# Optimization experiments

Measured on AMD Instinct MI355X. Metric: run time of the kernel, lower is better.

## Reference

```python
import jax, jax.numpy as jnp
import numpy as np

DIL = 1  # dilation (== padding for 3x3 stride-1)
KK = 9   # 3x3 kernel points


def setup_inputs() -> dict:
    key = jax.random.key(0)
    k1, k2, k3, k4 = jax.random.split(key, 4)
    B, C, H, W = 8, 64, 128, 128
    Cout = 64
    x = jax.random.normal(k1, (B, C, H, W), jnp.float32)
    # offset/mask conv: nn.Conv2d default init scale-ish; keep offsets moderate
    w_off = jax.random.normal(k2, (27, C, 3, 3), jnp.float32) * 0.02
    b_off = jax.random.uniform(k3, (27,), jnp.float32, -0.05, 0.05)
    # c2_msra_fill: std = sqrt(2 / (fan_in + fan_out)), fan_in = C*9
    std = float(np.sqrt(2.0 / (C * 9 + Cout)))
    w_dcn = jax.random.normal(k4, (Cout, C, 3, 3), jnp.float32) * std
    return {"x": x, "w_off": w_off, "b_off": b_off, "w_dcn": w_dcn}


def _conv3x3(x, w, b, dil):
    out = jax.lax.conv_general_dilated(
        x, w, window_strides=(1, 1), padding=[(dil, dil), (dil, dil)],
        rhs_dilation=(dil, dil), dimension_numbers=("NCHW", "OIHW", "NCHW"))
    return out + b[None, :, None, None]


def reference(x, w_off, b_off, w_dcn):
    B, C, H, W = x.shape
    Cout = w_dcn.shape[0]
    # offset/mask conv, chunk into offset_x / offset_y / mask, cat offsets
    om = _conv3x3(x, w_off, b_off, DIL)                  # [B,27,H,W]
    off_x, off_y, mask = jnp.split(om, 3, axis=1)        # each [B,9,H,W]
    offset = jnp.concatenate([off_x, off_y], axis=1)     # [B,18,H,W]
    mask = jax.nn.sigmoid(mask)                          # [B,9,H,W]
    # mmcv DCNv2 layout: offset channel 2k = dy_k, 2k+1 = dx_k
    off = offset.reshape(B, KK, 2, H, W)
    dy, dx = off[:, :, 0], off[:, :, 1]                  # [B,9,H,W]
    # base sampling grid: p = out_pos - pad + k*dil (stride 1, pad = dil)
    ky, kx = jnp.meshgrid(jnp.arange(3), jnp.arange(3), indexing="ij")
    ky = ky.reshape(KK).astype(jnp.float32)
    kx = kx.reshape(KK).astype(jnp.float32)
    base_y = (jnp.arange(H, dtype=jnp.float32)[None, :, None]
              - DIL + ky[:, None, None] * DIL)           # [9,H,1]
    base_x = (jnp.arange(W, dtype=jnp.float32)[None, None, :]
              - DIL + kx[:, None, None] * DIL)           # [9,1,W]
    py = dy + base_y[None]                               # [B,9,H,W]
    px = dx + base_x[None]
    # bilinear sample with zero padding outside the image
    y0 = jnp.floor(py)
    x0 = jnp.floor(px)
    xf = x.reshape(B, C, H * W)
    sampled = jnp.zeros((B, C, KK, H, W), x.dtype)
    for oy in (0.0, 1.0):
        for ox in (0.0, 1.0):
            yi = y0 + oy
            xi = x0 + ox
            wgt = (1.0 - jnp.abs(py - yi)) * (1.0 - jnp.abs(px - xi))
            valid = (yi >= 0) & (yi < H) & (xi >= 0) & (xi < W)
            yc = jnp.clip(yi, 0, H - 1).astype(jnp.int32)
            xc = jnp.clip(xi, 0, W - 1).astype(jnp.int32)
            idx = (yc * W + xc).reshape(B, KK * H * W)
            vals = jax.vmap(lambda f, i: jnp.take(f, i, axis=1))(xf, idx)
            vals = vals.reshape(B, C, KK, H, W)
            sampled = sampled + vals * (wgt * valid)[:, None]
    sampled = sampled * mask[:, None]                    # modulation
    # weighted reduction == conv with gathered patches
    out = jnp.einsum("bckhw,ock->bohw", sampled, w_dcn.reshape(Cout, C, KK))
    return out
```

## Files before the change

kernel.cpp:

```cpp
#include <hip/hip_runtime.h>
#include <math.h>

#define B_  8
#define C_  64
#define H_  128
#define W_  128
#define KK_ 9
#define CO_ 64
#define HW_ (H_*W_)
#define CK_ 576

typedef _Float16 f16x8 __attribute__((ext_vector_type(8)));
typedef _Float16 h2    __attribute__((ext_vector_type(2)));
typedef __attribute__((ext_vector_type(4))) float f32x4;

__device__ inline unsigned pkrtz(float a, float b){
    auto v = __builtin_amdgcn_cvt_pkrtz(a, b);
    union{decltype(v) h; unsigned u;} c; c.h = v; return c.u;
}
__device__ inline h2 u2h(unsigned u){ union{unsigned x; h2 h;} c; c.x = u; return c.h; }
__device__ inline unsigned h2u(h2 v){ union{h2 h; unsigned u;} c; c.h = v; return c.u; }
__device__ inline unsigned short f2h(float f){
    _Float16 h = (_Float16)f;
    union{_Float16 h; unsigned short s;} c; c.h = h; return c.s;
}
__device__ inline h2 bcast_lo(unsigned u){ return u2h(__builtin_amdgcn_perm(u, u, 0x01000100)); }
__device__ inline h2 bcast_hi(unsigned u){ return u2h(__builtin_amdgcn_perm(u, u, 0x03020302)); }

__global__ __launch_bounds__(256) void transpose_prep(
    const float* __restrict__ x, unsigned short* __restrict__ xt,
    const float* __restrict__ w_dcn, const float* __restrict__ w_off,
    unsigned short* __restrict__ w_bf, unsigned short* __restrict__ wA)
{
    __shared__ unsigned tb[64 * 33];
    if (blockIdx.x >= B_ * 256) {
        int i = (blockIdx.x - B_ * 256) * 256 + threadIdx.x;
        if (i < 64 * CK_) {
            int o = i / CK_, r = i % CK_;
            int tap = r >> 6, c = r & 63;
            w_bf[i] = f2h(w_dcn[o * CK_ + c * 9 + tap]);
        } else {
            int j = i - 64 * CK_;
            int o = j / CK_, r = j % CK_;
            int tap = r >> 6, c = r & 63;
            float v = (o < 27) ? w_off[o * CK_ + c * 9 + tap] : 0.f;
            wA[j] = f2h(v);
        }
        return;
    }
    int b = blockIdx.x >> 8;
    int pixbase = (blockIdx.x & 255) * 64;
    int t = threadIdx.x;
    #pragma unroll
    for (int i = 0; i < 2; ++i) {
        int idx = i * 256 + t;
        int cp = idx >> 4;
        int p4 = (idx & 15) * 4;
        const float* r0 = x + ((size_t)(b * C_) + 2 * cp    ) * HW_ + pixbase + p4;
        const float* r1 = x + ((size_t)(b * C_) + 2 * cp + 1) * HW_ + pixbase + p4;
        float4 f0 = *(const float4*)r0;
        float4 f1 = *(const float4*)r1;
        tb[(p4 + 0) * 33 + cp] = pkrtz(f0.x, f1.x);
        tb[(p4 + 1) * 33 + cp] = pkrtz(f0.y, f1.y);
        tb[(p4 + 2) * 33 + cp] = pkrtz(f0.z, f1.z);
        tb[(p4 + 3) * 33 + cp] = pkrtz(f0.w, f1.w);
    }
    __syncthreads();
    unsigned* xo = (unsigned*)xt + ((size_t)b * HW_ + pixbase) * 32;
    #pragma unroll
    for (int i = 0; i < 2; ++i) {
        int idx = i * 256 + t;
        int pix = idx >> 3, j = idx & 7;
        uint4 v;
        v.x = tb[pix * 33 + j * 4 + 0];
        v.y = tb[pix * 33 + j * 4 + 1];
        v.z = tb[pix * 33 + j * 4 + 2];
        v.w = tb[pix * 33 + j * 4 + 3];
        *(uint4*)(xo + pix * 32 + j * 4) = v;
    }
}

#define PXB 144
#define ROWB (66 * PXB)
#define SSTR4 400

__global__ __launch_bounds__(256, 4) void dcn15(
    const unsigned short* __restrict__ xt,
    const unsigned short* __restrict__ wA,
    const float* __restrict__ b_off,
    const unsigned short* __restrict__ w_bf,
    float* __restrict__ out)
{
    __shared__ __align__(16) unsigned char xrow[3 * ROWB];
    __shared__ uint2 scr_w[576];
    __shared__ int   scr_o[576];
    float* om = (float*)xrow;
    unsigned char* sS = xrow;

    int tile = blockIdx.x;
    int b  = tile >> 8;
    int p0 = (tile & 255) * 64;
    int y  = p0 >> 7;
    int x0 = p0 & 127;
    int t  = threadIdx.x;
    int lane = t & 63, w = t >> 6;
    int m = lane & 15, q = lane >> 4;

    const unsigned short* xbr = xt + (size_t)(b * HW_) * 64;

    for (int i = t; i < 3 * 66 * 8; i += 256) {
        int r = i / 528;
        int rem = i - r * 528;
        int c = rem >> 3;
        int g = rem & 7;
        int yy = y - 1 + r;
        int xx = x0 - 1 + c;
        uint4 v = {0, 0, 0, 0};
        if (yy >= 0 && yy < H_ && xx >= 0 && xx < W_)
            v = *(const uint4*)(xbr + ((size_t)yy * W_ + xx) * 64 + g * 8);
        *(uint4*)(xrow + r * ROWB + c * PXB + g * 16) = v;
    }
    __syncthreads();

    {
        int o0c = (w & 1) * 16;
        int pxh = (w >> 1) * 32;

        f32x4 accc[2] = {};
        #pragma unroll
        for (int ky = 0; ky < 3; ++ky) {
            #pragma unroll
            for (int kx = 0; kx < 3; ++kx) {
                int s2 = (ky * 3 + kx) * 2;
                f16x8 A0 = *(const f16x8*)(wA + (o0c + m) * CK_ + s2 * 32 + q * 8);
                f16x8 A1 = *(const f16x8*)(wA + (o0c + m) * CK_ + (s2 + 1) * 32 + q * 8);
                #pragma unroll
                for (int nt = 0; nt < 2; ++nt) {
                    int c = pxh + nt * 16 + m + kx;
                    const unsigned char* p = xrow + ky * ROWB + c * PXB + q * 16;
                    f16x8 b0 = *(const f16x8*)p;
                    f16x8 b1 = *(const f16x8*)(p + 64);
                    accc[nt] = __builtin_amdgcn_mfma_f32_16x16x32_f16(A0, b0, accc[nt], 0, 0, 0);
                    accc[nt] = __builtin_amdgcn_mfma_f32_16x16x32_f16(A1, b1, accc[nt], 0, 0, 0);
                }
            }
        }
        __syncthreads();
        #pragma unroll
        for (int nt = 0; nt < 2; ++nt) {
            #pragma unroll
            for (int r = 0; r < 4; ++r) {
                int j = o0c + q * 4 + r;
                if (j < 27)
                    om[j * 65 + pxh + nt * 16 + m] = accc[nt][r] + b_off[j];
            }
        }
    }
    __syncthreads();

    for (int i = t; i < 576; i += 256) {
        int k = i >> 6, sp = i & 63;
        float dy = om[(2 * k)     * 65 + sp];
        float dx = om[(2 * k + 1) * 65 + sp];
        float mk = 1.f / (1.f + __expf(-om[(18 + k) * 65 + sp]));
        float py = dy + (float)(y - 1 + k / 3);
        float px = dx + (float)(x0 + sp - 1 + k % 3);
        float fy = floorf(py), fx = floorf(px);
        int iy = (int)fy, ix = (int)fx;
        float ay = py - fy, ax = px - fx;
        float wy0 = (iy >= 0  && iy < H_)     ? (1.f - ay) : 0.f;
        float wy1 = (iy >= -1 && iy < H_ - 1) ? ay         : 0.f;
        float wx0 = (ix >= 0  && ix < W_)     ? (1.f - ax) : 0.f;
        float wx1 = (ix >= -1 && ix < W_ - 1) ? ax         : 0.f;
        int iy0 = min(max(iy, 0), H_ - 1);
        int iy1 = min(max(iy + 1, 0), H_ - 1);
        int ix0 = min(max(ix, 0), W_ - 1);
        int ix1 = min(max(ix + 1, 0), W_ - 1);
        float w00 = wy0*wx0*mk, w01 = wy0*wx1*mk, w10 = wy1*wx0*mk, w11 = wy1*wx1*mk;
        uint2 wv;
        wv.x = pkrtz(w00, w01);
        wv.y = pkrtz(w10, w11);
        scr_w[i] = wv;
        int off00 = (iy0 * W_ + ix0) * 128;
        scr_o[i] = off00 | ((ix1 != ix0) << 22) | ((iy1 != iy0) << 23);
    }

    int o0 = w * 16;
    __syncthreads();

    int cq = lane & 7;
    int g  = lane >> 3;
    const unsigned char* xb = (const unsigned char*)xbr;
    f32x4 acc[4] = {};
    int piB = w * 8 + g;

    uint2 wA_, wB_; int pB_;
    uint4 a00, a01, a10, a11;
    {
        wA_ = scr_w[piB];      int oo = scr_o[piB];
        wB_ = scr_w[piB + 32]; pB_ = scr_o[piB + 32];
        const unsigned char* a0 = xb + (oo & 0x3FFFFF) + cq * 16;
        int dxb = (oo >> 15) & 128;
        int dyb = (oo >> 9)  & 16384;
        a00 = *(const uint4*)(a0);
        a01 = *(const uint4*)(a0 + dxb);
        a10 = *(const uint4*)(a0 + dyb);
        a11 = *(const uint4*)(a0 + dyb + dxb);
    }

    #pragma unroll
    for (int chunk = 0; chunk < 3; ++chunk) {
        #pragma unroll
        for (int it6 = 0; it6 < 6; ++it6) {
            const int k = chunk * 6 + it6;
            uint2 wC_ = {}; int pC_ = 0;
            if (k + 2 < 18) {
                int P = piB + (k + 2) * 32;
                wC_ = scr_w[P]; pC_ = scr_o[P];
            }
            uint4 n00 = {}, n01 = {}, n10 = {}, n11 = {};
            if (k + 1 < 18) {
                const unsigned char* a0 = xb + (pB_ & 0x3FFFFF) + cq * 16;
                int dxb = (pB_ >> 15) & 128;
                int dyb = (pB_ >> 9)  & 16384;
                n00 = *(const uint4*)(a0);
                n01 = *(const uint4*)(a0 + dxb);
                n10 = *(const uint4*)(a0 + dyb);
                n11 = *(const uint4*)(a0 + dyb + dxb);
            }
            h2 w00 = bcast_lo(wA_.x), w01 = bcast_hi(wA_.x);
            h2 w10 = bcast_lo(wA_.y), w11 = bcast_hi(wA_.y);
            uint4 o4; h2 r;
            r = w00*u2h(a00.x) + w01*u2h(a01.x) + w10*u2h(a10.x) + w11*u2h(a11.x); o4.x = h2u(r);
            r = w00*u2h(a00.y) + w01*u2h(a01.y) + w10*u2h(a10.y) + w11*u2h(a11.y); o4.y = h2u(r);
            r = w00*u2h(a00.z) + w01*u2h(a01.z) + w10*u2h(a10.z) + w11*u2h(a11.z); o4.z = h2u(r);
            r = w00*u2h(a00.w) + w01*u2h(a01.w) + w10*u2h(a10.w) + w11*u2h(a11.w); o4.w = h2u(r);
            int sp  = (piB + (k & 1) * 32) & 63;
            int ktl = it6 >> 1;
            *(uint4*)&sS[sp * SSTR4 + ktl * 128 + cq * 16] = o4;
            wA_ = wB_; wB_ = wC_; pB_ = pC_;
            a00 = n00; a01 = n01; a10 = n10; a11 = n11;
        }
        f16x8 Af[6];
        #pragma unroll
        for (int s = 0; s < 6; ++s)
            Af[s] = *(const f16x8*)(w_bf + (o0 + m) * CK_ + (chunk * 6 + s) * 32 + q * 8);
        __syncthreads();

        #pragma unroll
        for (int s = 0; s < 6; ++s) {
            #pragma unroll
            for (int nt = 0; nt < 4; ++nt) {
                f16x8 bb = *(const f16x8*)&sS[(nt * 16 + m) * SSTR4 + s * 64 + q * 16];
                acc[nt] = __builtin_amdgcn_mfma_f32_16x16x32_f16(Af[s], bb, acc[nt], 0, 0, 0);
            }
        }
        __syncthreads();
    }

    #pragma unroll
    for (int nt = 0; nt < 4; ++nt) {
        #pragma unroll
        for (int r = 0; r < 4; ++r) {
            int o = o0 + q * 4 + r;
            out[((size_t)(b * CO_ + o)) * HW_ + p0 + nt * 16 + m] = acc[nt][r];
        }
    }
}

extern "C" void kernel_launch(void* const* d_in, const int* in_sizes, int n_in,
                              void* d_out, int out_size, void* d_ws, size_t ws_size,
                              hipStream_t stream)
{
    const float* x     = (const float*)d_in[0];
    const float* w_off = (const float*)d_in[1];
    const float* b_off = (const float*)d_in[2];
    const float* w_dcn = (const float*)d_in[3];
    float* out = (float*)d_out;

    unsigned short* xt   = (unsigned short*)d_ws;
    unsigned short* w_bf = xt + (size_t)B_ * HW_ * 64;
    unsigned short* wA   = w_bf + 64 * CK_;

    transpose_prep<<<B_ * 256 + 216, 256, 0, stream>>>(x, xt, w_dcn, w_off, w_bf, wA);
    dcn15<<<B_ * 256, 256, 0, stream>>>(xt, wA, b_off, w_bf, out);
}
```

Baseline: 146.2 us.

## Warp-specialize DCN main loop into gather producers and MFMA consumers with LDS flags

Replaces the block-wide gather-then-MFMA loop with warp specialization. Two wavefronts gather and bilinearly combine the sampled patches for each of the 9 taps into a triple-buffered LDS ring. The other two wavefronts run the MFMA reduction over 32 output channels each, and the two sides synchronize through LDS counter flags with spin-wait and sleep instead of __syncthreads. The goal is to overlap the gather latency with matrix-core work and remove the block-wide barriers. The cost is half as many waves doing the gathers, spin-wait overhead, and reliance on LDS ordering for correctness.

```diff
diff --git a/kernel.cpp b/kernel.cpp
--- a/kernel.cpp
+++ b/kernel.cpp
@@ -26,6 +26,15 @@
 }
 __device__ inline h2 bcast_lo(unsigned u){ return u2h(__builtin_amdgcn_perm(u, u, 0x01000100)); }
 __device__ inline h2 bcast_hi(unsigned u){ return u2h(__builtin_amdgcn_perm(u, u, 0x03020302)); }
+
+__device__ inline void lds_wait2(const volatile int* p){
+    while (*p < 2) __builtin_amdgcn_s_sleep(2);
+    asm volatile("" ::: "memory");
+}
+__device__ inline void lds_signal(int* p, int lane){
+    asm volatile("s_waitcnt lgkmcnt(0)" ::: "memory");
+    if (lane == 0) atomicAdd(p, 1);
+}
 
 __global__ __launch_bounds__(256) void transpose_prep(
     const float* __restrict__ x, unsigned short* __restrict__ xt,
@@ -80,11 +89,13 @@
     }
 }
 
+
 #define PXB 144
 #define ROWB (66 * PXB)
-#define SSTR4 400
-
-__global__ __launch_bounds__(256, 4) void dcn15(
+#define SSTRB 144
+#define SBUF (64 * SSTRB)
+
+__global__ __launch_bounds__(256, 4) void dcn19(
     const unsigned short* __restrict__ xt,
     const unsigned short* __restrict__ wA,
     const float* __restrict__ b_off,
@@ -94,6 +105,8 @@
     __shared__ __align__(16) unsigned char xrow[3 * ROWB];
     __shared__ uint2 scr_w[576];
     __shared__ int   scr_o[576];
+    __shared__ int   pflag[9];
+    __shared__ int   cflag[9];
     float* om = (float*)xrow;
     unsigned char* sS = xrow;
 
@@ -184,86 +197,83 @@
         int off00 = (iy0 * W_ + ix0) * 128;
         scr_o[i] = off00 | ((ix1 != ix0) << 22) | ((iy1 != iy0) << 23);
     }
-
-    int o0 = w * 16;
+    if (t < 9) { pflag[t] = 0; cflag[t] = 0; }
     __syncthreads();
 
     int cq = lane & 7;
     int g  = lane >> 3;
     const unsigned char* xb = (const unsigned char*)xbr;
-    f32x4 acc[4] = {};
-    int piB = w * 8 + g;
-
-    uint2 wA_, wB_; int pB_;
-    uint4 a00, a01, a10, a11;
-    {
-        wA_ = scr_w[piB];      int oo = scr_o[piB];
-        wB_ = scr_w[piB + 32]; pB_ = scr_o[piB + 32];
-        const unsigned char* a0 = xb + (oo & 0x3FFFFF) + cq * 16;
-        int dxb = (oo >> 15) & 128;
-        int dyb = (oo >> 9)  & 16384;
-        a00 = *(const uint4*)(a0);
-        a01 = *(const uint4*)(a0 + dxb);
-        a10 = *(const uint4*)(a0 + dyb);
-        a11 = *(const uint4*)(a0 + dyb + dxb);
-    }
-
-    #pragma unroll
-    for (int chunk = 0; chunk < 3; ++chunk) {
-        #pragma unroll
-        for (int it6 = 0; it6 < 6; ++it6) {
-            const int k = chunk * 6 + it6;
-            uint2 wC_ = {}; int pC_ = 0;
-            if (k + 2 < 18) {
-                int P = piB + (k + 2) * 32;
-                wC_ = scr_w[P]; pC_ = scr_o[P];
-            }
-            uint4 n00 = {}, n01 = {}, n10 = {}, n11 = {};
-            if (k + 1 < 18) {
-                const unsigned char* a0 = xb + (pB_ & 0x3FFFFF) + cq * 16;
-                int dxb = (pB_ >> 15) & 128;
-                int dyb = (pB_ >> 9)  & 16384;
-                n00 = *(const uint4*)(a0);
-                n01 = *(const uint4*)(a0 + dxb);
-                n10 = *(const uint4*)(a0 + dyb);
-                n11 = *(const uint4*)(a0 + dyb + dxb);
-            }
-            h2 w00 = bcast_lo(wA_.x), w01 = bcast_hi(wA_.x);
-            h2 w10 = bcast_lo(wA_.y), w11 = bcast_hi(wA_.y);
-            uint4 o4; h2 r;
-            r = w00*u2h(a00.x) + w01*u2h(a01.x) + w10*u2h(a10.x) + w11*u2h(a11.x); o4.x = h2u(r);
-            r = w00*u2h(a00.y) + w01*u2h(a01.y) + w10*u2h(a10.y) + w11*u2h(a11.y); o4.y = h2u(r);
-            r = w00*u2h(a00.z) + w01*u2h(a01.z) + w10*u2h(a10.z) + w11*u2h(a11.z); o4.z = h2u(r);
-            r = w00*u2h(a00.w) + w01*u2h(a01.w) + w10*u2h(a10.w) + w11*u2h(a11.w); o4.w = h2u(r);
-            int sp  = (piB + (k & 1) * 32) & 63;
-            int ktl = it6 >> 1;
-            *(uint4*)&sS[sp * SSTR4 + ktl * 128 + cq * 16] = o4;
-            wA_ = wB_; wB_ = wC_; pB_ = pC_;
-            a00 = n00; a01 = n01; a10 = n10; a11 = n11;
-        }
-        f16x8 Af[6];
-        #pragma unroll
-        for (int s = 0; s < 6; ++s)
-            Af[s] = *(const f16x8*)(w_bf + (o0 + m) * CK_ + (chunk * 6 + s) * 32 + q * 8);
-        __syncthreads();
-
-        #pragma unroll
-        for (int s = 0; s < 6; ++s) {
-            #pragma unroll
-            for (int nt = 0; nt < 4; ++nt) {
-                f16x8 bb = *(const f16x8*)&sS[(nt * 16 + m) * SSTR4 + s * 64 + q * 16];
-                acc[nt] = __builtin_amdgcn_mfma_f32_16x16x32_f16(Af[s], bb, acc[nt], 0, 0, 0);
-            }
-        }
-        __syncthreads();
-    }
-
-    #pragma unroll
-    for (int nt = 0; nt < 4; ++nt) {
-        #pragma unroll
-        for (int r = 0; r < 4; ++r) {
-            int o = o0 + q * 4 + r;
-            out[((size_t)(b * CO_ + o)) * HW_ + p0 + nt * 16 + m] = acc[nt][r];
+
+    if (w < 2) {
+        #pragma unroll
+        for (int t9 = 0; t9 < 9; ++t9) {
+            if (t9 >= 3) lds_wait2(&cflag[t9 - 3]);
+            unsigned char* sb = sS + (t9 % 3) * SBUF;
+            #pragma unroll
+            for (int u = 0; u < 4; ++u) {
+                int sp = w * 32 + g * 4 + u;
+                int P  = t9 * 64 + sp;
+                uint2 wv = scr_w[P];
+                int   oo = scr_o[P];
+                const unsigned char* a0 = xb + (oo & 0x3FFFFF) + cq * 16;
+                int dxb = (oo >> 15) & 128;
+                int dyb = (oo >> 9)  & 16384;
+                uint4 a00 = *(const uint4*)(a0);
+                uint4 a01 = *(const uint4*)(a0 + dxb);
+                uint4 a10 = *(const uint4*)(a0 + dyb);
+                uint4 a11 = *(const uint4*)(a0 + dyb + dxb);
+                h2 w00 = bcast_lo(wv.x), w01 = bcast_hi(wv.x);
+                h2 w10 = bcast_lo(wv.y), w11 = bcast_hi(wv.y);
+                uint4 o4; h2 r;
+                r = w00*u2h(a00.x) + w01*u2h(a01.x) + w10*u2h(a10.x) + w11*u2h(a11.x); o4.x = h2u(r);
+                r = w00*u2h(a00.y) + w01*u2h(a01.y) + w10*u2h(a10.y) + w11*u2h(a11.y); o4.y = h2u(r);
+                r = w00*u2h(a00.z) + w01*u2h(a01.z) + w10*u2h(a10.z) + w11*u2h(a11.z); o4.z = h2u(r);
+                r = w00*u2h(a00.w) + w01*u2h(a01.w) + w10*u2h(a10.w) + w11*u2h(a11.w); o4.w = h2u(r);
+                *(uint4*)&sb[sp * SSTRB + cq * 16] = o4;
+            }
+            lds_signal(&pflag[t9], lane);
+        }
+        return;
+    }
+
+    int o0c2 = (w - 2) * 32;
+    f32x4 acc2[2][4] = {};
+
+    #pragma unroll
+    for (int t9 = 0; t9 < 9; ++t9) {
+        const unsigned short* wb = w_bf + (o0c2 + m) * CK_ + (2 * t9) * 32 + q * 8;
+        f16x8 Af00 = *(const f16x8*)(wb);
+        f16x8 Af01 = *(const f16x8*)(wb + 32);
+        f16x8 Af10 = *(const f16x8*)(wb + 16 * CK_);
+        f16x8 Af11 = *(const f16x8*)(wb + 16 * CK_ + 32);
+
+        lds_wait2(&pflag[t9]);
+        const unsigned char* sb = sS + (t9 % 3) * SBUF;
+
+        #pragma unroll
+        for (int nt = 0; nt < 4; ++nt) {
+            f16x8 bb0 = *(const f16x8*)&sb[(nt * 16 + m) * SSTRB + q * 16];
+            acc2[0][nt] = __builtin_amdgcn_mfma_f32_16x16x32_f16(Af00, bb0, acc2[0][nt], 0, 0, 0);
+            acc2[1][nt] = __builtin_amdgcn_mfma_f32_16x16x32_f16(Af10, bb0, acc2[1][nt], 0, 0, 0);
+        }
+        #pragma unroll
+        for (int nt = 0; nt < 4; ++nt) {
+            f16x8 bb1 = *(const f16x8*)&sb[(nt * 16 + m) * SSTRB + 64 + q * 16];
+            acc2[0][nt] = __builtin_amdgcn_mfma_f32_16x16x32_f16(Af01, bb1, acc2[0][nt], 0, 0, 0);
+            acc2[1][nt] = __builtin_amdgcn_mfma_f32_16x16x32_f16(Af11, bb1, acc2[1][nt], 0, 0, 0);
+        }
+        lds_signal(&cflag[t9], lane);
+    }
+
+    #pragma unroll
+    for (int jo = 0; jo < 2; ++jo) {
+        #pragma unroll
+        for (int nt = 0; nt < 4; ++nt) {
+            #pragma unroll
+            for (int r = 0; r < 4; ++r) {
+                int o = o0c2 + jo * 16 + q * 4 + r;
+                out[((size_t)(b * CO_ + o)) * HW_ + p0 + nt * 16 + m] = acc2[jo][nt][r];
+            }
         }
     }
 }
@@ -283,5 +293,5 @@
     unsigned short* wA   = w_bf + 64 * CK_;
 
     transpose_prep<<<B_ * 256 + 216, 256, 0, stream>>>(x, xt, w_dcn, w_off, w_bf, wA);
-    dcn15<<<B_ * 256, 256, 0, stream>>>(xt, wA, b_off, w_bf, out);
-}
+    dcn19<<<B_ * 256, 256, 0, stream>>>(xt, wA, b_off, w_bf, out);
+}
```

Measured after the change: 147.1 us. No clear change (+0.6%).
